# Performance work log

Hardware: AMD Instinct MI355X
Metric: run time of the kernel (lower is better)

Reference implementation:

```python
import jax, jax.numpy as jnp
import numpy as np

B, T, F, U, L = 64, 700, 3, 400, 3


def setup_inputs() -> dict:
    key = jax.random.key(0)
    ks = jax.random.split(key, 10)
    s = 0.08  # small init to keep gates unsaturated
    return {
        "x": jax.random.normal(ks[0], (B, T, F), jnp.float32),
        "Wx0": jax.random.normal(ks[1], (F, 4 * U), jnp.float32) * s,
        "Wx1": jax.random.normal(ks[2], (U, 4 * U), jnp.float32) * s,
        "Wx2": jax.random.normal(ks[3], (U, 4 * U), jnp.float32) * s,
        "Wh": jax.random.normal(ks[4], (L, U, 4 * U), jnp.float32) * s,
        "b": jnp.zeros((L, 4 * U), jnp.float32),
        "pi": jax.random.normal(ks[5], (L, U), jnp.float32) * s,
        "pf": jax.random.normal(ks[6], (L, U), jnp.float32) * s,
        "po": jax.random.normal(ks[7], (L, U), jnp.float32) * s,
        "Wd": jax.random.normal(ks[8], (U, F), jnp.float32) * s,
        "bd": jnp.zeros((F,), jnp.float32),
    }


def _lstm_peephole_layer(x_tbd, Wx, Wh_l, b_l, pi_l, pf_l, po_l):
    """x_tbd: [T, B, D] -> [T, B, U] with peephole LSTM (Graves 2013)."""
    Bsz = x_tbd.shape[1]
    Uu = Wh_l.shape[0]
    # Precompute the input contribution for all timesteps in one GEMM.
    xp = jnp.einsum("tbd,dk->tbk", x_tbd, Wx) + b_l  # [T, B, 4U]

    def step(carry, zt):
        h, c = carry
        z = zt + h @ Wh_l  # [B, 4U]
        zi, zf, zg, zo = jnp.split(z, 4, axis=-1)
        i = jax.nn.sigmoid(zi + pi_l * c)
        f = jax.nn.sigmoid(zf + pf_l * c)
        c_new = f * c + i * jnp.tanh(zg)
        o = jax.nn.sigmoid(zo + po_l * c_new)
        h_new = o * jnp.tanh(c_new)
        return (h_new, c_new), h_new

    init = (jnp.zeros((Bsz, Uu), x_tbd.dtype), jnp.zeros((Bsz, Uu), x_tbd.dtype))
    _, hs = jax.lax.scan(step, init, xp)
    return hs  # [T, B, U]


def reference(x, Wx0, Wx1, Wx2, Wh, b, pi, pf, po, Wd, bd):
    h = jnp.transpose(x, (1, 0, 2))  # [T, B, F]
    for l, Wx in enumerate((Wx0, Wx1, Wx2)):
        h = _lstm_peephole_layer(h, Wx, Wh[l], b[l], pi[l], pf[l], po[l])
    out = jnp.einsum("tbu,uf->tbf", h, Wd) + bd
    return jnp.transpose(out, (1, 0, 2))  # [B, T, F]
```

## Files before the change

kernel.cpp:

```cpp
#include <hip/hip_runtime.h>
#include <hip/hip_fp16.h>
#include <math.h>

#define B_ 64
#define T_ 700
#define U_ 400
#define NF 704
#define FR_LS 13312

typedef _Float16 half8 __attribute__((ext_vector_type(8)));
typedef float float4v __attribute__((ext_vector_type(4)));

union AFrag { unsigned u[4]; half8 h; };

__device__ __forceinline__ unsigned agloadu(const unsigned* p) {
    return __hip_atomic_load(p, __ATOMIC_RELAXED, __HIP_MEMORY_SCOPE_AGENT);
}
__device__ __forceinline__ void agstoreu(unsigned* p, unsigned v) {
    __hip_atomic_store(p, v, __ATOMIC_RELAXED, __HIP_MEMORY_SCOPE_AGENT);
}
__device__ __forceinline__ float sig_(float v) {
    return __builtin_amdgcn_rcpf(1.f + __expf(-v));
}
__device__ __forceinline__ float tanh_(float v) {
    return 1.f - 2.f * __builtin_amdgcn_rcpf(__expf(2.f * v) + 1.f);
}
__device__ __forceinline__ void waitflag(const unsigned* f, unsigned target) {
    while (agloadu(f) < target) __builtin_amdgcn_s_sleep(2);
}
__device__ __forceinline__ unsigned f16u(float v) {
    union { _Float16 f; unsigned short s; } cv; cv.f = (_Float16)v; return (unsigned)cv.s;
}

__device__ __forceinline__ void pollfrag13(const unsigned* __restrict__ base,
                                           const unsigned par,
                                           AFrag* __restrict__ a, const int lane)
{
    {
        const unsigned* pp = base + (lane % 13) * 256 + ((lane * 37) & 255);
        while (!__all((int)(((agloadu(pp) ^ par) & 1u) == 0u)))
            __builtin_amdgcn_s_sleep(3);
    }
    unsigned pend = 0x1FFFu;
    do {
#pragma unroll
        for (int ck = 0; ck < 13; ++ck) if ((pend >> ck) & 1) {
#pragma unroll
            for (int d = 0; d < 4; ++d)
                a[ck].u[d] = agloadu(base + ck * 256 + d * 64 + lane);
        }
#pragma unroll
        for (int ck = 0; ck < 13; ++ck) if ((pend >> ck) & 1) {
            const unsigned m = (a[ck].u[0] ^ par) | (a[ck].u[1] ^ par)
                             | (a[ck].u[2] ^ par) | (a[ck].u[3] ^ par);
            if (__all((int)((m & 1u) == 0u))) pend &= ~(1u << ck);
        }
        if (pend) __builtin_amdgcn_s_sleep(3);
    } while (pend);
}

template<int DEPTH, int CP>
__global__ void __launch_bounds__(256, 1)
lstm_mix(const float* __restrict__ x,
         const float* __restrict__ Wx0,
         const float* __restrict__ Wx1,
         const float* __restrict__ Wx2,
         const float* __restrict__ Wh,
         const float* __restrict__ bias,
         const float* __restrict__ pi,
         const float* __restrict__ pf,
         const float* __restrict__ po,
         const float* __restrict__ Wd,
         const float* __restrict__ bd,
         float* __restrict__ out,
         unsigned* __restrict__ ws)
{
    __shared__ alignas(16) _Float16 wlds[26 * 512];
    __shared__ alignas(16) float zlds[4 * 528];
    __shared__ float gc[160];

    const int LW = NF * CP * 32;
    unsigned* F0 = ws;
    unsigned* F1 = F0 + LW;
    unsigned* F2 = F1 + LW;
    unsigned* FO = F2 + LW;
    unsigned* frag0 = ws + (size_t)4 * LW;

    const int blk  = blockIdx.x;
    const int tid  = threadIdx.x;
    const int lane = tid & 63;
    const int wv   = tid >> 6;
    const int cpi  = (blk + wv) & (CP - 1);

    int layer, u0;
    if      (blk < 50)  { layer = 0; u0 = blk * 8; }
    else if (blk < 150) { layer = 1; u0 = (blk - 50) * 4; }
    else if (blk < 250) { layer = 2; u0 = (blk - 150) * 4; }
    else                { layer = 3; u0 = 0; }

    const bool padw = (blk == 49) || (blk == 149) || (blk == 249);
    int pad_off[2];
    {
        const int i0 = tid, i1 = tid + 256;
        pad_off[0] = (i0 >> 7) * 3328 + 12 * 256 + (((i0 >> 4) & 3) * 64)
                   + (2 + ((i0 >> 6) & 1)) * 16 + (i0 & 15);
        pad_off[1] = (i1 >> 7) * 3328 + 12 * 256 + (((i1 >> 4) & 3) * 64)
                   + (2 + ((i1 >> 6) & 1)) * 16 + (i1 & 15);
    }

    {
        const float* __restrict__ Wxl = (layer == 1) ? Wx1 : Wx2;
        for (int i = tid; i < 26 * 64; i += 256) {
            const int ln = i & 63, ck = i >> 6;
            const int q = ln >> 4, nn = ln & 15;
            float vals[8];
#pragma unroll
            for (int j = 0; j < 8; ++j) {
                const int kc = ck % 13;
                const int k = kc * 32 + q * 8 + j;
                float v = 0.f;
                if (k < 400) {
                    if (layer == 0) {
                        const int col32 = (ck / 13) * 16 + nn;
                        const int gcol = (col32 >> 3) * U_ + u0 + (col32 & 7);
                        v = Wh[(size_t)k * 1600 + gcol];
                    } else if (layer < 3) {
                        const int gcol = (nn >> 2) * U_ + u0 + (nn & 3);
                        v = (ck >= 13) ? Wh[((size_t)layer * U_ + k) * 1600 + gcol]
                                       : Wxl[(size_t)k * 1600 + gcol];
                    } else {
                        if (ck < 13 && nn < 3) v = Wd[k * 3 + nn];
                    }
                }
                vals[j] = v;
            }
#pragma unroll
            for (int j = 0; j < 8; ++j)
                wlds[ck * 512 + ln * 8 + j] = (_Float16)vals[j];
        }
        if (layer == 0) {
            if (tid < 128) {
                const int col32 = tid >> 2, comp = tid & 3;
                const int gcol = (col32 >> 3) * U_ + u0 + (col32 & 7);
                gc[tid] = (comp == 0) ? bias[gcol] : Wx0[(size_t)(comp - 1) * 1600 + gcol];
            } else if (tid < 152) {
                const int idx = tid - 128, ul = idx / 3, j = idx - ul * 3;
                const float* pp = (j == 0) ? pi : (j == 1) ? pf : po;
                gc[tid] = pp[u0 + ul];
            }
        } else if (layer < 3) {
            if (tid < 16) {
                gc[tid] = bias[layer * 1600 + (tid >> 2) * U_ + u0 + (tid & 3)];
            } else if (tid < 28) {
                const int idx = tid - 16, ul = idx / 3, j = idx - ul * 3;
                const float* pp = (j == 0) ? pi : (j == 1) ? pf : po;
                gc[tid] = pp[layer * U_ + u0 + ul];
            }
        } else {
            if (tid < 3) gc[tid] = bd[tid];
        }
    }
    __syncthreads();

    const int wvz   = wv * 528;
    const int b_loc = lane & 15;
    const int quad  = lane >> 4;
    float cst[2] = {0.f, 0.f};

    for (int t = 0; t < T_; ++t) {
        const int sw = t % DEPTH;
        const int sr = (t + DEPTH - 1) % DEPTH;
        const unsigned pI = (unsigned)((t / DEPTH) & 1);
        const unsigned pO = (unsigned)(((t - 1) / DEPTH) & 1);

        float x0, x1, x2;
        if (layer == 0) {
            const size_t xb = (size_t)(wv * 16 + b_loc) * T_ + t;
            x0 = x[xb * 3 + 0]; x1 = x[xb * 3 + 1]; x2 = x[xb * 3 + 2];
        }

        if (lane == 0) {
            if (layer == 0) {
                if (wv == 0 && t >= DEPTH) waitflag(F1 + ((t - DEPTH) * CP + cpi) * 32, 100);
            } else if (layer == 1) {
                waitflag(F0 + (t * CP + cpi) * 32, 50);
                if (wv == 0 && t >= DEPTH) waitflag(F2 + ((t - DEPTH) * CP + cpi) * 32, 100);
            } else if (layer == 2) {
                waitflag(F1 + (t * CP + cpi) * 32, 100);
                if (wv == 0 && t >= DEPTH) waitflag(FO + ((t - DEPTH) * CP + cpi) * 32, 1);
            } else {
                waitflag(F2 + (t * CP + cpi) * 32, 100);
            }
        }
        asm volatile("" ::: "memory");

        AFrag ainp[13];
        if (layer == 1 || layer == 2) {
            const unsigned* frI = frag0 + (size_t)((layer - 1) * DEPTH + sw) * FR_LS + wv * 3328;
#pragma unroll
            for (int kc = 0; kc < 13; ++kc)
#pragma unroll
                for (int d = 0; d < 4; ++d)
                    ainp[kc].u[d] = agloadu(frI + kc * 256 + d * 64 + lane);
        }

        AFrag aown[13];
        if (layer == 3) {
            const unsigned* frI = frag0 + (size_t)(2 * DEPTH + sw) * FR_LS + wv * 3328;
#pragma unroll
            for (int kc = 0; kc < 13; ++kc)
#pragma unroll
                for (int d = 0; d < 4; ++d)
                    aown[kc].u[d] = agloadu(frI + kc * 256 + d * 64 + lane);
        } else if (t >= 1) {
            const unsigned* frO = frag0 + (size_t)(layer * DEPTH + sr) * FR_LS + wv * 3328;
            pollfrag13(frO, pO, aown, lane);
        } else {
#pragma unroll
            for (int kc = 0; kc < 13; ++kc)
#pragma unroll
                for (int d = 0; d < 4; ++d) aown[kc].u[d] = 0u;
        }
        asm volatile("" ::: "memory");

        if (layer == 0) {
            float4v acc0 = {0.f, 0.f, 0.f, 0.f}, acc1 = {0.f, 0.f, 0.f, 0.f};
#pragma unroll
            for (int kc = 0; kc < 13; ++kc) {
                const half8 w0 = *(const half8*)&wlds[kc * 512 + lane * 8];
                const half8 w1 = *(const half8*)&wlds[(13 + kc) * 512 + lane * 8];
                acc0 = __builtin_amdgcn_mfma_f32_16x16x32_f16(aown[kc].h, w0, acc0, 0, 0, 0);
                acc1 = __builtin_amdgcn_mfma_f32_16x16x32_f16(aown[kc].h, w1, acc1, 0, 0, 0);
            }
#pragma unroll
            for (int r = 0; r < 4; ++r) {
                zlds[wvz + (quad * 4 + r) * 33 + b_loc] = acc0[r];
                zlds[wvz + (quad * 4 + r) * 33 + 16 + b_loc] = acc1[r];
            }
        } else if (layer < 3) {
            float4v acc = {0.f, 0.f, 0.f, 0.f};
#pragma unroll
            for (int kc = 0; kc < 13; ++kc) {
                const half8 wA = *(const half8*)&wlds[kc * 512 + lane * 8];
                const half8 wB = *(const half8*)&wlds[(13 + kc) * 512 + lane * 8];
                acc = __builtin_amdgcn_mfma_f32_16x16x32_f16(ainp[kc].h, wA, acc, 0, 0, 0);
                acc = __builtin_amdgcn_mfma_f32_16x16x32_f16(aown[kc].h, wB, acc, 0, 0, 0);
            }
#pragma unroll
            for (int r = 0; r < 4; ++r)
                zlds[wvz + (quad * 4 + r) * 33 + b_loc] = acc[r];
        } else {
            float4v acc = {0.f, 0.f, 0.f, 0.f};
#pragma unroll
            for (int kc = 0; kc < 13; ++kc) {
                const half8 w0 = *(const half8*)&wlds[kc * 512 + lane * 8];
                acc = __builtin_amdgcn_mfma_f32_16x16x32_f16(aown[kc].h, w0, acc, 0, 0, 0);
            }
            if (b_loc < 3) {
#pragma unroll
                for (int r = 0; r < 4; ++r)
                    out[((size_t)(wv * 16 + quad * 4 + r) * T_ + t) * 3 + b_loc] = acc[r] + gc[b_loc];
            }
        }
        __syncthreads();

        if (padw) {
            unsigned* fr_dst = frag0 + (size_t)(layer * DEPTH + sw) * FR_LS;
            agstoreu(fr_dst + pad_off[0], pI);
            agstoreu(fr_dst + pad_off[1], pI);
        }

        if (layer == 0) {
            unsigned* fr_dst = frag0 + (size_t)(0 * DEPTH + sw) * FR_LS + wv * 3328;
#pragma unroll
            for (int q = 0; q < 2; ++q) {
                const int ul = q * 4 + quad;
                const int ug = u0 + ul;
                float z[4];
#pragma unroll
                for (int g = 0; g < 4; ++g) {
                    const int gb = (g * 8 + ul) * 4;
                    z[g] = zlds[wvz + b_loc * 33 + g * 8 + ul]
                         + gc[gb + 0] + x0 * gc[gb + 1] + x1 * gc[gb + 2] + x2 * gc[gb + 3];
                }
                const float cp = cst[q];
                const float ig = sig_(z[0] + gc[128 + ul * 3 + 0] * cp);
                const float fg = sig_(z[1] + gc[128 + ul * 3 + 1] * cp);
                const float cn = fg * cp + ig * tanh_(z[2]);
                const float og = sig_(z[3] + gc[128 + ul * 3 + 2] * cn);
                cst[q] = cn;
                const float hv = og * tanh_(cn);
                const float pv = __shfl_xor(hv, 16, 64);
                if ((quad & 1) == 0) {
                    const unsigned pw_ = ((f16u(hv) & ~1u) | pI) | (f16u(pv) << 16);
                    const int u = ug;
                    agstoreu(fr_dst + (u >> 5) * 256 + ((u & 7) >> 1) * 64
                                    + ((u >> 3) & 3) * 16 + b_loc, pw_);
                }
            }
        } else if (layer < 3) {
            unsigned* fr_dst = frag0 + (size_t)(layer * DEPTH + sw) * FR_LS + wv * 3328;
            const int ul = quad;
            float z[4];
#pragma unroll
            for (int g = 0; g < 4; ++g)
                z[g] = zlds[wvz + b_loc * 33 + g * 4 + ul] + gc[g * 4 + ul];
            const float cp = cst[0];
            const float ig = sig_(z[0] + gc[16 + ul * 3 + 0] * cp);
            const float fg = sig_(z[1] + gc[16 + ul * 3 + 1] * cp);
            const float cn = fg * cp + ig * tanh_(z[2]);
            const float og = sig_(z[3] + gc[16 + ul * 3 + 2] * cn);
            cst[0] = cn;
            const float hv = og * tanh_(cn);
            const float pv = __shfl_xor(hv, 16, 64);
            if ((ul & 1) == 0) {
                const unsigned pw_ = ((f16u(hv) & ~1u) | pI) | (f16u(pv) << 16);
                const int u = u0 + ul;
                agstoreu(fr_dst + (u >> 5) * 256 + ((u & 7) >> 1) * 64
                                + ((u >> 3) & 3) * 16 + b_loc, pw_);
            }
        }

        asm volatile("s_waitcnt vmcnt(0)" ::: "memory");
        __syncthreads();
        if (tid < CP) {
            unsigned* f = (layer == 0) ? F0 : (layer == 1) ? F1
                        : (layer == 2) ? F2 : FO;
            __hip_atomic_fetch_add(f + (t * CP + tid) * 32, 1u,
                                   __ATOMIC_RELAXED, __HIP_MEMORY_SCOPE_AGENT);
        }
    }
}

template<int DEPTH, int CP>
static void launch_variant(void* const* d_in, float* out, unsigned* ws, hipStream_t stream) {
    const float* x    = (const float*)d_in[0];
    const float* Wx0  = (const float*)d_in[1];
    const float* Wx1  = (const float*)d_in[2];
    const float* Wx2  = (const float*)d_in[3];
    const float* Wh   = (const float*)d_in[4];
    const float* bias = (const float*)d_in[5];
    const float* pi   = (const float*)d_in[6];
    const float* pf   = (const float*)d_in[7];
    const float* po   = (const float*)d_in[8];
    const float* Wd   = (const float*)d_in[9];
    const float* bd   = (const float*)d_in[10];
    void* args[] = { (void*)&x, (void*)&Wx0, (void*)&Wx1, (void*)&Wx2, (void*)&Wh,
                     (void*)&bias, (void*)&pi, (void*)&pf, (void*)&po,
                     (void*)&Wd, (void*)&bd, (void*)&out, (void*)&ws };
    hipError_t err = hipLaunchCooperativeKernel((void*)lstm_mix<DEPTH, CP>,
                                                dim3(251), dim3(256), args, 0, stream);
    if (err != hipSuccess)
        hipLaunchKernelGGL((lstm_mix<DEPTH, CP>), dim3(251), dim3(256), 0, stream,
                           x, Wx0, Wx1, Wx2, Wh, bias, pi, pf, po, Wd, bd, out, ws);
}

extern "C" void kernel_launch(void* const* d_in, const int* in_sizes, int n_in,
                              void* d_out, int out_size, void* d_ws, size_t ws_size,
                              hipStream_t stream) {
    float* out = (float*)d_out;
    unsigned* ws = (unsigned*)d_ws;

    auto flagbytes = [](int cp) -> size_t { return (size_t)4 * NF * cp * 32 * 4; };
    auto fragbytes = [](int depth) -> size_t { return (size_t)3 * depth * FR_LS * 4; };

    if (ws_size >= flagbytes(8) + fragbytes(8)) {
        hipMemsetAsync(d_ws, 0, flagbytes(8), stream);
        hipMemsetAsync((char*)d_ws + flagbytes(8), 0xFF, fragbytes(8), stream);
        launch_variant<8, 8>(d_in, out, ws, stream);
    } else if (ws_size >= flagbytes(4) + fragbytes(4)) {
        hipMemsetAsync(d_ws, 0, flagbytes(4), stream);
        hipMemsetAsync((char*)d_ws + flagbytes(4), 0xFF, fragbytes(4), stream);
        launch_variant<4, 4>(d_in, out, ws, stream);
    } else {
        hipMemsetAsync(d_ws, 0, flagbytes(2), stream);
        hipMemsetAsync((char*)d_ws + flagbytes(2), 0xFF, fragbytes(2), stream);
        launch_variant<2, 2>(d_in, out, ws, stream);
    }
}
```

Before: 2.844 ms.

## Replace per-step counter flags with parity-polled fragments and a single ring-slot counter

Drops the per-timestep atomic counter flags and the block-wide barriers around them. Consumers now poll the parity bits embedded in the fp16 fragment words for both their own layer's recurrent input and the previous layer's output. Only one representative block per layer publishes a progress counter, which guards ring-buffer reuse. Poll sleep intervals are shortened as well. The aim is to cut inter-block synchronization latency on the serial recurrence critical path. The cost is more spinning loads, and correctness now rests on the parity protocol and on the single-block counter holding for every block.

Measured after the change: 4.350 ms. 1.53x slower.

```diff
diff --git a/kernel.cpp b/kernel.cpp
--- a/kernel.cpp
+++ b/kernel.cpp
@@ -5,7 +5,6 @@
 #define B_ 64
 #define T_ 700
 #define U_ 400
-#define NF 704
 #define FR_LS 13312
 
 typedef _Float16 half8 __attribute__((ext_vector_type(8)));
@@ -25,13 +24,14 @@
 __device__ __forceinline__ float tanh_(float v) {
     return 1.f - 2.f * __builtin_amdgcn_rcpf(__expf(2.f * v) + 1.f);
 }
-__device__ __forceinline__ void waitflag(const unsigned* f, unsigned target) {
+__device__ __forceinline__ void waitctr(const unsigned* f, unsigned target) {
     while (agloadu(f) < target) __builtin_amdgcn_s_sleep(2);
 }
 __device__ __forceinline__ unsigned f16u(float v) {
     union { _Float16 f; unsigned short s; } cv; cv.f = (_Float16)v; return (unsigned)cv.s;
 }
 
+template<int SL>
 __device__ __forceinline__ void pollfrag13(const unsigned* __restrict__ base,
                                            const unsigned par,
                                            AFrag* __restrict__ a, const int lane)
@@ -39,7 +39,7 @@
     {
         const unsigned* pp = base + (lane % 13) * 256 + ((lane * 37) & 255);
         while (!__all((int)(((agloadu(pp) ^ par) & 1u) == 0u)))
-            __builtin_amdgcn_s_sleep(3);
+            __builtin_amdgcn_s_sleep(SL);
     }
     unsigned pend = 0x1FFFu;
     do {
@@ -55,42 +55,37 @@
                              | (a[ck].u[2] ^ par) | (a[ck].u[3] ^ par);
             if (__all((int)((m & 1u) == 0u))) pend &= ~(1u << ck);
         }
-        if (pend) __builtin_amdgcn_s_sleep(3);
+        if (pend) __builtin_amdgcn_s_sleep(1);
     } while (pend);
 }
 
-template<int DEPTH, int CP>
+template<int DEPTH>
 __global__ void __launch_bounds__(256, 1)
-lstm_mix(const float* __restrict__ x,
-         const float* __restrict__ Wx0,
-         const float* __restrict__ Wx1,
-         const float* __restrict__ Wx2,
-         const float* __restrict__ Wh,
-         const float* __restrict__ bias,
-         const float* __restrict__ pi,
-         const float* __restrict__ pf,
-         const float* __restrict__ po,
-         const float* __restrict__ Wd,
-         const float* __restrict__ bd,
-         float* __restrict__ out,
-         unsigned* __restrict__ ws)
+lstm_pb(const float* __restrict__ x,
+        const float* __restrict__ Wx0,
+        const float* __restrict__ Wx1,
+        const float* __restrict__ Wx2,
+        const float* __restrict__ Wh,
+        const float* __restrict__ bias,
+        const float* __restrict__ pi,
+        const float* __restrict__ pf,
+        const float* __restrict__ po,
+        const float* __restrict__ Wd,
+        const float* __restrict__ bd,
+        float* __restrict__ out,
+        unsigned* __restrict__ ws)
 {
     __shared__ alignas(16) _Float16 wlds[26 * 512];
     __shared__ alignas(16) float zlds[4 * 528];
     __shared__ float gc[160];
 
-    const int LW = NF * CP * 32;
-    unsigned* F0 = ws;
-    unsigned* F1 = F0 + LW;
-    unsigned* F2 = F1 + LW;
-    unsigned* FO = F2 + LW;
-    unsigned* frag0 = ws + (size_t)4 * LW;
+    unsigned* Dc    = ws;
+    unsigned* frag0 = ws + 512;
 
     const int blk  = blockIdx.x;
     const int tid  = threadIdx.x;
     const int lane = tid & 63;
     const int wv   = tid >> 6;
-    const int cpi  = (blk + wv) & (CP - 1);
 
     int layer, u0;
     if      (blk < 50)  { layer = 0; u0 = blk * 8; }
@@ -99,14 +94,6 @@
     else                { layer = 3; u0 = 0; }
 
     const bool padw = (blk == 49) || (blk == 149) || (blk == 249);
-    int pad_off[2];
-    {
-        const int i0 = tid, i1 = tid + 256;
-        pad_off[0] = (i0 >> 7) * 3328 + 12 * 256 + (((i0 >> 4) & 3) * 64)
-                   + (2 + ((i0 >> 6) & 1)) * 16 + (i0 & 15);
-        pad_off[1] = (i1 >> 7) * 3328 + 12 * 256 + (((i1 >> 4) & 3) * 64)
-                   + (2 + ((i1 >> 6) & 1)) * 16 + (i1 & 15);
-    }
 
     {
         const float* __restrict__ Wxl = (layer == 1) ? Wx1 : Wx2;
@@ -179,47 +166,23 @@
             x0 = x[xb * 3 + 0]; x1 = x[xb * 3 + 1]; x2 = x[xb * 3 + 2];
         }
 
-        if (lane == 0) {
-            if (layer == 0) {
-                if (wv == 0 && t >= DEPTH) waitflag(F1 + ((t - DEPTH) * CP + cpi) * 32, 100);
-            } else if (layer == 1) {
-                waitflag(F0 + (t * CP + cpi) * 32, 50);
-                if (wv == 0 && t >= DEPTH) waitflag(F2 + ((t - DEPTH) * CP + cpi) * 32, 100);
-            } else if (layer == 2) {
-                waitflag(F1 + (t * CP + cpi) * 32, 100);
-                if (wv == 0 && t >= DEPTH) waitflag(FO + ((t - DEPTH) * CP + cpi) * 32, 1);
+        AFrag aown[13], ainp[13];
+        if (layer < 3) {
+            if (t >= 1) {
+                pollfrag13<1>(frag0 + (size_t)(layer * DEPTH + sr) * FR_LS + wv * 3328,
+                              pO, aown, lane);
             } else {
-                waitflag(F2 + (t * CP + cpi) * 32, 100);
-            }
-        }
-        asm volatile("" ::: "memory");
-
-        AFrag ainp[13];
-        if (layer == 1 || layer == 2) {
-            const unsigned* frI = frag0 + (size_t)((layer - 1) * DEPTH + sw) * FR_LS + wv * 3328;
-#pragma unroll
-            for (int kc = 0; kc < 13; ++kc)
-#pragma unroll
-                for (int d = 0; d < 4; ++d)
-                    ainp[kc].u[d] = agloadu(frI + kc * 256 + d * 64 + lane);
-        }
-
-        AFrag aown[13];
-        if (layer == 3) {
-            const unsigned* frI = frag0 + (size_t)(2 * DEPTH + sw) * FR_LS + wv * 3328;
-#pragma unroll
-            for (int kc = 0; kc < 13; ++kc)
-#pragma unroll
-                for (int d = 0; d < 4; ++d)
-                    aown[kc].u[d] = agloadu(frI + kc * 256 + d * 64 + lane);
-        } else if (t >= 1) {
-            const unsigned* frO = frag0 + (size_t)(layer * DEPTH + sr) * FR_LS + wv * 3328;
-            pollfrag13(frO, pO, aown, lane);
+#pragma unroll
+                for (int ck = 0; ck < 13; ++ck)
+#pragma unroll
+                    for (int d = 0; d < 4; ++d) aown[ck].u[d] = 0u;
+            }
+            if (layer >= 1)
+                pollfrag13<2>(frag0 + (size_t)((layer - 1) * DEPTH + sw) * FR_LS + wv * 3328,
+                              pI, ainp, lane);
         } else {
-#pragma unroll
-            for (int kc = 0; kc < 13; ++kc)
-#pragma unroll
-                for (int d = 0; d < 4; ++d) aown[kc].u[d] = 0u;
+            pollfrag13<2>(frag0 + (size_t)(2 * DEPTH + sw) * FR_LS + wv * 3328,
+                          pI, aown, lane);
         }
         asm volatile("" ::: "memory");
 
@@ -262,12 +225,15 @@
                     out[((size_t)(wv * 16 + quad * 4 + r) * T_ + t) * 3 + b_loc] = acc[r] + gc[b_loc];
             }
         }
-        __syncthreads();
+
+        if (layer < 3 && lane == 0 && t >= DEPTH)
+            waitctr(Dc + (layer * 4 + wv) * 32, (unsigned)(t - DEPTH + 2));
+        asm volatile("" ::: "memory");
 
         if (padw) {
-            unsigned* fr_dst = frag0 + (size_t)(layer * DEPTH + sw) * FR_LS;
-            agstoreu(fr_dst + pad_off[0], pI);
-            agstoreu(fr_dst + pad_off[1], pI);
+            unsigned* fd = frag0 + (size_t)(layer * DEPTH + sw) * FR_LS + wv * 3328 + 12 * 256;
+            agstoreu(fd + (lane >> 4) * 64 + 32 + (lane & 15), pI);
+            agstoreu(fd + (lane >> 4) * 64 + 48 + (lane & 15), pI);
         }
 
         if (layer == 0) {
@@ -321,18 +287,15 @@
             }
         }
 
-        asm volatile("s_waitcnt vmcnt(0)" ::: "memory");
-        __syncthreads();
-        if (tid < CP) {
-            unsigned* f = (layer == 0) ? F0 : (layer == 1) ? F1
-                        : (layer == 2) ? F2 : FO;
-            __hip_atomic_fetch_add(f + (t * CP + tid) * 32, 1u,
-                                   __ATOMIC_RELAXED, __HIP_MEMORY_SCOPE_AGENT);
+        if (lane == 0) {
+            if      (blk == 50)  agstoreu(Dc + (0 * 4 + wv) * 32, (unsigned)(t + 1));
+            else if (blk == 150) agstoreu(Dc + (1 * 4 + wv) * 32, (unsigned)(t + 1));
+            else if (blk == 250) agstoreu(Dc + (2 * 4 + wv) * 32, (unsigned)(t + 1));
         }
     }
 }
 
-template<int DEPTH, int CP>
+template<int DEPTH>
 static void launch_variant(void* const* d_in, float* out, unsigned* ws, hipStream_t stream) {
     const float* x    = (const float*)d_in[0];
     const float* Wx0  = (const float*)d_in[1];
@@ -348,10 +311,10 @@
     void* args[] = { (void*)&x, (void*)&Wx0, (void*)&Wx1, (void*)&Wx2, (void*)&Wh,
                      (void*)&bias, (void*)&pi, (void*)&pf, (void*)&po,
                      (void*)&Wd, (void*)&bd, (void*)&out, (void*)&ws };
-    hipError_t err = hipLaunchCooperativeKernel((void*)lstm_mix<DEPTH, CP>,
+    hipError_t err = hipLaunchCooperativeKernel((void*)lstm_pb<DEPTH>,
                                                 dim3(251), dim3(256), args, 0, stream);
     if (err != hipSuccess)
-        hipLaunchKernelGGL((lstm_mix<DEPTH, CP>), dim3(251), dim3(256), 0, stream,
+        hipLaunchKernelGGL((lstm_pb<DEPTH>), dim3(251), dim3(256), 0, stream,
                            x, Wx0, Wx1, Wx2, Wh, bias, pi, pf, po, Wd, bd, out, ws);
 }
 
@@ -361,20 +324,15 @@
     float* out = (float*)d_out;
     unsigned* ws = (unsigned*)d_ws;
 
-    auto flagbytes = [](int cp) -> size_t { return (size_t)4 * NF * cp * 32 * 4; };
     auto fragbytes = [](int depth) -> size_t { return (size_t)3 * depth * FR_LS * 4; };
 
-    if (ws_size >= flagbytes(8) + fragbytes(8)) {
-        hipMemsetAsync(d_ws, 0, flagbytes(8), stream);
-        hipMemsetAsync((char*)d_ws + flagbytes(8), 0xFF, fragbytes(8), stream);
-        launch_variant<8, 8>(d_in, out, ws, stream);
-    } else if (ws_size >= flagbytes(4) + fragbytes(4)) {
-        hipMemsetAsync(d_ws, 0, flagbytes(4), stream);
-        hipMemsetAsync((char*)d_ws + flagbytes(4), 0xFF, fragbytes(4), stream);
-        launch_variant<4, 4>(d_in, out, ws, stream);
+    if (ws_size >= 2048 + fragbytes(8)) {
+        hipMemsetAsync(d_ws, 0, 2048, stream);
+        hipMemsetAsync((char*)d_ws + 2048, 0xFF, fragbytes(8), stream);
+        launch_variant<8>(d_in, out, ws, stream);
     } else {
-        hipMemsetAsync(d_ws, 0, flagbytes(2), stream);
-        hipMemsetAsync((char*)d_ws + flagbytes(2), 0xFF, fragbytes(2), stream);
-        launch_variant<2, 2>(d_in, out, ws, stream);
+        hipMemsetAsync(d_ws, 0, 2048, stream);
+        hipMemsetAsync((char*)d_ws + 2048, 0xFF, fragbytes(4), stream);
+        launch_variant<4>(d_in, out, ws, stream);
     }
 }
```
